# Kernel tuning notes

Hardware: AMD Instinct MI355X
Metric: run time of the kernel (lower is better)

Reference implementation:

```python
import jax, jax.numpy as jnp
import numpy as np

N = 100000      # nodes
E = 1600000     # edges (avg degree 16)
F_IN = 64       # input features
HID = 16        # ChebConv hidden (fixed in source)
C = 40          # num_classes
K = 2           # Chebyshev order (fixed in source)
LAMBDA_MAX = 2.0  # PyG ChebConv default


def setup_inputs() -> dict:
    key = jax.random.key(0)
    ks = jax.random.split(key, 6)
    x = jax.random.normal(ks[0], (N, F_IN), dtype=jnp.float32)
    edge_index = jax.random.randint(ks[1], (2, E), 0, N, dtype=jnp.int32)
    edge_weight = jax.random.uniform(ks[2], (E,), dtype=jnp.float32)
    W1 = jax.random.normal(ks[3], (K, F_IN, HID), dtype=jnp.float32) / np.float32(np.sqrt(F_IN))
    b1 = jnp.zeros((HID,), dtype=jnp.float32)
    W2 = jax.random.normal(ks[4], (K, HID, C), dtype=jnp.float32) / np.float32(np.sqrt(HID))
    b2 = jnp.zeros((C,), dtype=jnp.float32)
    return {"x": x, "edge_weight": edge_weight, "W1": W1, "b1": b1,
            "W2": W2, "b2": b2, "edge_index": edge_index}


def _cheb_norm(src, dst, edge_weight):
    # deg from symmetric normalization (aggregate at dst, PyG col)
    deg = jax.ops.segment_sum(edge_weight, dst, num_segments=N)
    dinv = jnp.where(deg > 0, jax.lax.rsqrt(jnp.maximum(deg, 1e-30)), 0.0)
    # Lhat = 2L/lambda_max - I ; with L = I - A_norm -> edge weight = -(2/lmax)*A_norm
    norm = -(2.0 / LAMBDA_MAX) * dinv[src] * edge_weight * dinv[dst]
    loop = 2.0 / LAMBDA_MAX - 1.0  # self-loop weight (0 for lambda_max=2)
    return norm, loop


def _cheb_conv(x, src, dst, norm, loop, W, b):
    # K=2: Tx0 = x, Tx1 = Lhat @ x (sparse gather-scale-scatter)
    Tx1 = jax.ops.segment_sum(norm[:, None] * x[src], dst, num_segments=N) + loop * x
    return jnp.einsum('nf,fo->no', x, W[0]) + jnp.einsum('nf,fo->no', Tx1, W[1]) + b


def reference(x, edge_weight, W1, b1, W2, b2, edge_index):
    src, dst = edge_index[0], edge_index[1]
    norm, loop = _cheb_norm(src, dst, edge_weight)
    h = jax.nn.relu(_cheb_conv(x, src, dst, norm, loop, W1, b1))
    # F.dropout with training=False is identity (inference reference)
    o = _cheb_conv(h, src, dst, norm, loop, W2, b2)
    return jax.nn.log_softmax(o, axis=1)
```

## Files before the change

### kernel.cpp

```cpp
#include <hip/hip_runtime.h>
#include <math.h>

#define NN 100000
#define NE 1600000
#define FIN 64
#define HID 16
#define NC 40

#define NG 512
#define GN 196
#define GCAP 3600
#define CH 4096
#define NBK ((NE + CH - 1) / CH)

typedef unsigned int u32;
typedef unsigned long long u64;
typedef unsigned short u16;

__device__ inline u16 f2bf(float f) {
    u32 u = __float_as_uint(f);
    return (u16)((u + 0x7FFF + ((u >> 16) & 1)) >> 16);
}
__device__ inline u32 pack2bf(float lo, float hi) {
    return (u32)f2bf(lo) | ((u32)f2bf(hi) << 16);
}

__global__ void k_zero(int* __restrict__ p) {
    p[blockIdx.x * 256 + threadIdx.x] = 0;
}

__global__ void __launch_bounds__(256) k_bucket(const int* __restrict__ src,
                                                const int* __restrict__ dst,
                                                const float* __restrict__ ew,
                                                int* __restrict__ bcur,
                                                u64* __restrict__ stg) {
    __shared__ u64 stage[CH];
    __shared__ int lcnt[NG];
    __shared__ int loff[NG];
    __shared__ int lcur[NG];
    __shared__ int gst[NG];
    __shared__ int ssum[256];
    __shared__ int totsh;
    int tid = threadIdx.x;
    int e0 = blockIdx.x * CH;
    for (int i = tid; i < NG; i += 256) lcnt[i] = 0;
    __syncthreads();
    u32 hb[16];
    #pragma unroll
    for (int k = 0; k < 16; ++k) {
        int e = e0 + k * 256 + tid;
        hb[k] = 0xFFFFFFFFu;
        if (e < NE) {
            int d = dst[e];
            int g = d / GN;
            hb[k] = ((u32)g << 16) | (u32)(d - g * GN);
            atomicAdd(&lcnt[g], 1);
        }
    }
    __syncthreads();
    int b0 = lcnt[2 * tid], b1c = lcnt[2 * tid + 1];
    int s = b0 + b1c;
    ssum[tid] = s;
    __syncthreads();
    #pragma unroll
    for (int off = 1; off < 256; off <<= 1) {
        int t = tid >= off ? ssum[tid - off] : 0;
        __syncthreads();
        ssum[tid] += t;
        __syncthreads();
    }
    int excl = ssum[tid] - s;
    loff[2 * tid] = excl;         loff[2 * tid + 1] = excl + b0;
    lcur[2 * tid] = excl;         lcur[2 * tid + 1] = excl + b0;
    gst[2 * tid]     = atomicAdd(&bcur[(2 * tid) << 4], b0);
    gst[2 * tid + 1] = atomicAdd(&bcur[(2 * tid + 1) << 4], b1c);
    if (tid == 255) totsh = ssum[255];
    __syncthreads();
    #pragma unroll
    for (int k = 0; k < 16; ++k) {
        if (hb[k] != 0xFFFFFFFFu) {
            int e = e0 + k * 256 + tid;
            int g = hb[k] >> 16;
            u32 q = (u32)fminf(ew[e] * 32767.f + 0.5f, 32767.f);
            u32 lo = (u32)src[e] | (q << 17);
            int slot = atomicAdd(&lcur[g], 1);
            stage[slot] = ((u64)hb[k] << 32) | (u64)lo;
        }
    }
    __syncthreads();
    int total = totsh;
    for (int i = tid; i < total; i += 256) {
        u64 r = stage[i];
        int g = (int)(r >> 48);
        int slot = gst[g] + (i - loff[g]);
        if (slot < GCAP) stg[(size_t)g * GCAP + slot] = r;
    }
}

__global__ void __launch_bounds__(256) k_build(const u64* __restrict__ stg,
                                               const int* __restrict__ bcur,
                                               int* __restrict__ row_ptr,
                                               float* __restrict__ dinv,
                                               u32* __restrict__ edges4) {
    __shared__ u64 lrec[GCAP];
    __shared__ u32 hc[GN];
    __shared__ u32 hw[GN];
    __shared__ int tsum[256];
    __shared__ int sb[NG];
    int g = blockIdx.x, tid = threadIdx.x;
    for (int i = tid; i < GN; i += 256) { hc[i] = 0; hw[i] = 0; }
    for (int i = tid; i < NG; i += 256) sb[i] = bcur[i << 4];
    __syncthreads();
    int n = sb[g];
    if (n > GCAP) n = GCAP;
    int b0 = sb[2 * tid], b1 = sb[2 * tid + 1];
    const u64* base = stg + (size_t)g * GCAP;
    for (int i = tid; i < n; i += 256) {
        u64 r = base[i];
        lrec[i] = r;
        int ld = (int)((r >> 32) & 0xFFFF);
        atomicAdd(&hc[ld], 1u);
        atomicAdd(&hw[ld], ((u32)r) >> 17);
    }
    __syncthreads();
    int s2 = b0 + b1;
    tsum[tid] = s2;
    __syncthreads();
    #pragma unroll
    for (int off = 1; off < 256; off <<= 1) {
        int t = tid >= off ? tsum[tid - off] : 0;
        __syncthreads();
        tsum[tid] += t;
        __syncthreads();
    }
    int excl = tsum[tid] - s2;
    sb[2 * tid] = excl; sb[2 * tid + 1] = excl + b0;
    __syncthreads();
    int gbase = sb[g];
    int c = (tid < GN) ? (int)hc[tid] : 0;
    tsum[tid] = c;
    __syncthreads();
    #pragma unroll
    for (int off = 1; off < 256; off <<= 1) {
        int t = tid >= off ? tsum[tid - off] : 0;
        __syncthreads();
        tsum[tid] += t;
        __syncthreads();
    }
    if (tid < GN) {
        int run = gbase + tsum[tid] - c;
        int nd = g * GN + tid;
        if (nd <= NN) {
            row_ptr[nd] = run;
            if (nd < NN) {
                float deg = (float)hw[tid] * (1.0f / 32767.0f);
                dinv[nd] = deg > 0.f ? rsqrtf(fmaxf(deg, 1e-30f)) : 0.f;
            }
        }
        hc[tid] = (u32)run;
    }
    __syncthreads();
    for (int i = tid; i < n; i += 256) {
        u64 r = lrec[i];
        int ld = (int)((r >> 32) & 0xFFFF);
        edges4[atomicAdd(&hc[ld], 1u)] = (u32)r;
    }
}

__global__ void __launch_bounds__(256) k_mm1(const float* __restrict__ x,
                                             const float* __restrict__ W1,
                                             const float* __restrict__ dinv,
                                             float* __restrict__ A1,
                                             u16* __restrict__ B0h) {
    __shared__ float4 w4[512];
    int tid = threadIdx.x;
    for (int i = tid; i < 512; i += 256) w4[i] = *(const float4*)(W1 + i * 4);
    __syncthreads();
    int sel = tid >> 7;
    int node = blockIdx.x * 128 + (tid & 127);
    if (node >= NN) return;
    const float4* xr = (const float4*)(x + node * FIN);
    const float4* wb = w4 + sel * 256;
    float4 a0 = {0,0,0,0}, a1 = {0,0,0,0}, a2 = {0,0,0,0}, a3 = {0,0,0,0};
    #pragma unroll
    for (int ft = 0; ft < 16; ++ft) {
        float4 xv = xr[ft];
        const float4* wf = wb + ft * 16;
        #pragma unroll
        for (int q = 0; q < 4; ++q) {
            float xs = q == 0 ? xv.x : q == 1 ? xv.y : q == 2 ? xv.z : xv.w;
            float4 w0 = wf[q * 4 + 0], w1v = wf[q * 4 + 1], w2v = wf[q * 4 + 2], w3v = wf[q * 4 + 3];
            a0.x += xs * w0.x; a0.y += xs * w0.y; a0.z += xs * w0.z; a0.w += xs * w0.w;
            a1.x += xs * w1v.x; a1.y += xs * w1v.y; a1.z += xs * w1v.z; a1.w += xs * w1v.w;
            a2.x += xs * w2v.x; a2.y += xs * w2v.y; a2.z += xs * w2v.z; a2.w += xs * w2v.w;
            a3.x += xs * w3v.x; a3.y += xs * w3v.y; a3.z += xs * w3v.z; a3.w += xs * w3v.w;
        }
    }
    if (sel == 0) {
        float4* o = (float4*)(A1 + node * HID);
        o[0] = a0; o[1] = a1; o[2] = a2; o[3] = a3;
    } else {
        float di = dinv[node];
        uint4 p0, p1;
        p0.x = pack2bf(a0.x * di, a0.y * di);
        p0.y = pack2bf(a0.z * di, a0.w * di);
        p0.z = pack2bf(a1.x * di, a1.y * di);
        p0.w = pack2bf(a1.z * di, a1.w * di);
        p1.x = pack2bf(a2.x * di, a2.y * di);
        p1.y = pack2bf(a2.z * di, a2.w * di);
        p1.z = pack2bf(a3.x * di, a3.y * di);
        p1.w = pack2bf(a3.z * di, a3.w * di);
        uint4* o = (uint4*)(B0h + node * HID);
        o[0] = p0; o[1] = p1;
    }
}

template <int MODE>
__global__ void k_gather(const int* __restrict__ row_ptr, const u32* __restrict__ edges4,
                         const u16* __restrict__ Bh,
                         const float* __restrict__ A1, const float* __restrict__ b1,
                         const float* __restrict__ dinv,
                         u32* __restrict__ o1, u32* __restrict__ o2) {
    int node = blockIdx.x * 4 + (threadIdx.x >> 6);
    int lane = threadIdx.x & 63;
    int slot = lane >> 3, q = lane & 7;
    if (node >= NN) return;
    int beg = row_ptr[node], end = row_ptr[node + 1];
    const u32* Bw = (const u32*)Bh;
    float accL = 0.f, accH = 0.f;
    int p0 = beg + slot;
    if (end - beg <= 16) {
        u32 r0 = (p0 < end) ? edges4[p0] : 0u;
        u32 r1 = (p0 + 8 < end) ? edges4[p0 + 8] : 0u;
        u32 c0 = Bw[(r0 & 0x1FFFF) * 8 + q];
        u32 c1 = Bw[(r1 & 0x1FFFF) * 8 + q];
        float w0 = (float)(r0 >> 17), w1 = (float)(r1 >> 17);
        accL = w0 * __uint_as_float(c0 << 16) + w1 * __uint_as_float(c1 << 16);
        accH = w0 * __uint_as_float(c0 & 0xFFFF0000u) + w1 * __uint_as_float(c1 & 0xFFFF0000u);
    } else {
        u32 r[4];
        #pragma unroll
        for (int k = 0; k < 4; ++k) {
            int p = p0 + 8 * k;
            r[k] = (p < end) ? edges4[p] : 0u;
        }
        #pragma unroll
        for (int k = 0; k < 4; ++k) {
            u32 c = Bw[(r[k] & 0x1FFFF) * 8 + q];
            float w = (float)(r[k] >> 17);
            accL += w * __uint_as_float(c << 16);
            accH += w * __uint_as_float(c & 0xFFFF0000u);
        }
        for (int p = p0 + 32; p < end; p += 8) {
            u32 rr = edges4[p];
            u32 c = Bw[(rr & 0x1FFFF) * 8 + q];
            float w = (float)(rr >> 17);
            accL += w * __uint_as_float(c << 16);
            accH += w * __uint_as_float(c & 0xFFFF0000u);
        }
    }
    #pragma unroll
    for (int m = 8; m < 64; m <<= 1) {
        accL += __shfl_xor(accL, m, 64);
        accH += __shfl_xor(accH, m, 64);
    }
    if (slot == 0) {
        float di = dinv[node];
        float sc = di * (1.0f / 32767.0f);
        int f = 2 * q;
        if (MODE == 0) {
            float2 a = *(const float2*)(A1 + node * HID + f);
            float2 bb = *(const float2*)(b1 + f);
            float hL = fmaxf(a.x - sc * accL + bb.x, 0.f);
            float hH = fmaxf(a.y - sc * accH + bb.y, 0.f);
            o1[node * 8 + q] = pack2bf(hL, hH);
            o2[node * 8 + q] = pack2bf(hL * di, hH * di);
        } else {
            o1[node * 8 + q] = pack2bf(-sc * accL, -sc * accH);
        }
    }
}

__global__ void __launch_bounds__(256) k_mm2_lsm(const u32* __restrict__ hb,
                                                 const u32* __restrict__ Tb,
                                                 const float* __restrict__ W2,
                                                 const float* __restrict__ b2,
                                                 float* __restrict__ out) {
    __shared__ float4 w4[32][10];
    __shared__ float sb2[NC];
    int tid = threadIdx.x;
    for (int i = tid; i < 320; i += 256) {
        int f = i / 10, ct = i % 10;
        w4[f][ct] = *(const float4*)(W2 + f * 40 + ct * 4);
    }
    for (int i = tid; i < NC; i += 256) sb2[i] = b2[i];
    __syncthreads();
    int node = blockIdx.x * 256 + tid;
    if (node >= NN) return;
    float v[32];
    uint4 ha = ((const uint4*)(hb + node * 8))[0];
    uint4 hbq = ((const uint4*)(hb + node * 8))[1];
    uint4 ta = ((const uint4*)(Tb + node * 8))[0];
    uint4 tbq = ((const uint4*)(Tb + node * 8))[1];
    u32 hw_[8] = {ha.x, ha.y, ha.z, ha.w, hbq.x, hbq.y, hbq.z, hbq.w};
    u32 tw_[8] = {ta.x, ta.y, ta.z, ta.w, tbq.x, tbq.y, tbq.z, tbq.w};
    #pragma unroll
    for (int qq = 0; qq < 8; ++qq) {
        v[2 * qq]     = __uint_as_float(hw_[qq] << 16);
        v[2 * qq + 1] = __uint_as_float(hw_[qq] & 0xFFFF0000u);
        v[16 + 2 * qq]     = __uint_as_float(tw_[qq] << 16);
        v[16 + 2 * qq + 1] = __uint_as_float(tw_[qq] & 0xFFFF0000u);
    }
    float lg[NC];
    #pragma unroll
    for (int ct = 0; ct < 10; ++ct) {
        float ax = sb2[ct * 4 + 0], ay = sb2[ct * 4 + 1], az = sb2[ct * 4 + 2], aw = sb2[ct * 4 + 3];
        #pragma unroll
        for (int f = 0; f < 32; ++f) {
            float4 wv = w4[f][ct];
            ax += v[f] * wv.x; ay += v[f] * wv.y; az += v[f] * wv.z; aw += v[f] * wv.w;
        }
        lg[ct * 4 + 0] = ax; lg[ct * 4 + 1] = ay; lg[ct * 4 + 2] = az; lg[ct * 4 + 3] = aw;
    }
    float m = lg[0];
    #pragma unroll
    for (int c = 1; c < NC; ++c) m = fmaxf(m, lg[c]);
    float sum = 0.f;
    #pragma unroll
    for (int c = 0; c < NC; ++c) sum += __expf(lg[c] - m);
    float lse = m + __logf(sum);
    float* orow = out + node * NC;
    #pragma unroll
    for (int ct = 0; ct < 10; ++ct) {
        float4 r;
        r.x = lg[ct * 4 + 0] - lse; r.y = lg[ct * 4 + 1] - lse;
        r.z = lg[ct * 4 + 2] - lse; r.w = lg[ct * 4 + 3] - lse;
        *(float4*)(orow + ct * 4) = r;
    }
}

extern "C" void kernel_launch(void* const* d_in, const int* in_sizes, int n_in,
                              void* d_out, int out_size, void* d_ws, size_t ws_size,
                              hipStream_t stream) {
    const float* x  = (const float*)d_in[0];
    const float* ew = (const float*)d_in[1];
    const float* W1 = (const float*)d_in[2];
    const float* b1 = (const float*)d_in[3];
    const float* W2 = (const float*)d_in[4];
    const float* b2 = (const float*)d_in[5];
    const int*   ei = (const int*)d_in[6];
    const int* src = ei;
    const int* dst = ei + NE;
    float* out = (float*)d_out;

    const int NPAD = 100352;
    int*   bcur    = (int*)d_ws;
    u64*   stg     = (u64*)(bcur + NG * 16);
    u32*   edges4  = (u32*)(stg + (size_t)NG * GCAP);
    int*   row_ptr = (int*)(edges4 + NE);
    float* dinv    = (float*)(row_ptr + NPAD);
    float* A1      = dinv + NPAD;
    u16*   B0h     = (u16*)(A1 + NN * HID);
    u32*   hbf     = (u32*)(B0h + NN * HID);
    u32*   h2      = hbf + NN * 8;
    u32*   Tbf     = h2 + NN * 8;

    k_zero<<<NG * 16 / 256, 256, 0, stream>>>(bcur);
    k_bucket<<<NBK, 256, 0, stream>>>(src, dst, ew, bcur, stg);
    k_build<<<NG, 256, 0, stream>>>(stg, bcur, row_ptr, dinv, edges4);
    k_mm1<<<(NN + 127) / 128, 256, 0, stream>>>(x, W1, dinv, A1, B0h);
    k_gather<0><<<(NN + 3) / 4, 256, 0, stream>>>(row_ptr, edges4, B0h, A1, b1, dinv, hbf, h2);
    k_gather<1><<<(NN + 3) / 4, 256, 0, stream>>>(row_ptr, edges4, (const u16*)h2, nullptr, nullptr, dinv, Tbf, nullptr);
    k_mm2_lsm<<<(NN + 255) / 256, 256, 0, stream>>>(hbf, Tbf, W2, b2, out);
}
```

Measured before the change: 133.4 us.

## Fuse second-layer gather with output matmul and log-softmax per wavefront

Merges the second sparse gather and the final W2 matmul plus log_softmax into one kernel. Each 64-lane wavefront handles one node: 8 lanes hold features, 8 slots split the 40 classes, and shuffles perform the reductions. This removes the Tbf intermediate round-trip through memory and one kernel launch. In exchange, every block reloads W2 into shared memory (25k blocks, 1280 floats each), adds shuffle reductions, and writes output as scattered 4-byte stores instead of float4.

```diff
diff --git a/kernel.cpp b/kernel.cpp
--- a/kernel.cpp
+++ b/kernel.cpp
@@ -215,12 +215,11 @@
     }
 }
 
-template <int MODE>
-__global__ void k_gather(const int* __restrict__ row_ptr, const u32* __restrict__ edges4,
-                         const u16* __restrict__ Bh,
-                         const float* __restrict__ A1, const float* __restrict__ b1,
-                         const float* __restrict__ dinv,
-                         u32* __restrict__ o1, u32* __restrict__ o2) {
+__global__ void k_gather0(const int* __restrict__ row_ptr, const u32* __restrict__ edges4,
+                          const u16* __restrict__ Bh,
+                          const float* __restrict__ A1, const float* __restrict__ b1,
+                          const float* __restrict__ dinv,
+                          u32* __restrict__ o1, u32* __restrict__ o2) {
     int node = blockIdx.x * 4 + (threadIdx.x >> 6);
     int lane = threadIdx.x & 63;
     int slot = lane >> 3, q = lane & 7;
@@ -268,75 +267,109 @@
         float di = dinv[node];
         float sc = di * (1.0f / 32767.0f);
         int f = 2 * q;
-        if (MODE == 0) {
-            float2 a = *(const float2*)(A1 + node * HID + f);
-            float2 bb = *(const float2*)(b1 + f);
-            float hL = fmaxf(a.x - sc * accL + bb.x, 0.f);
-            float hH = fmaxf(a.y - sc * accH + bb.y, 0.f);
-            o1[node * 8 + q] = pack2bf(hL, hH);
-            o2[node * 8 + q] = pack2bf(hL * di, hH * di);
-        } else {
-            o1[node * 8 + q] = pack2bf(-sc * accL, -sc * accH);
-        }
-    }
-}
-
-__global__ void __launch_bounds__(256) k_mm2_lsm(const u32* __restrict__ hb,
-                                                 const u32* __restrict__ Tb,
-                                                 const float* __restrict__ W2,
-                                                 const float* __restrict__ b2,
-                                                 float* __restrict__ out) {
-    __shared__ float4 w4[32][10];
-    __shared__ float sb2[NC];
+        float2 a = *(const float2*)(A1 + node * HID + f);
+        float2 bb = *(const float2*)(b1 + f);
+        float hL = fmaxf(a.x - sc * accL + bb.x, 0.f);
+        float hH = fmaxf(a.y - sc * accH + bb.y, 0.f);
+        o1[node * 8 + q] = pack2bf(hL, hH);
+        o2[node * 8 + q] = pack2bf(hL * di, hH * di);
+    }
+}
+
+__global__ void __launch_bounds__(256) k_gather_lsm(const int* __restrict__ row_ptr,
+                                                    const u32* __restrict__ edges4,
+                                                    const u16* __restrict__ Bh,
+                                                    const u32* __restrict__ hbf,
+                                                    const float* __restrict__ dinv,
+                                                    const float* __restrict__ W2,
+                                                    const float* __restrict__ b2,
+                                                    float* __restrict__ out) {
+    __shared__ float w2s[32 * 41];
+    __shared__ float b2s[NC];
     int tid = threadIdx.x;
-    for (int i = tid; i < 320; i += 256) {
-        int f = i / 10, ct = i % 10;
-        w4[f][ct] = *(const float4*)(W2 + f * 40 + ct * 4);
-    }
-    for (int i = tid; i < NC; i += 256) sb2[i] = b2[i];
-    __syncthreads();
-    int node = blockIdx.x * 256 + tid;
+    for (int i = tid; i < 1280; i += 256) {
+        int f = i / 40, c = i - f * 40;
+        w2s[f * 41 + c] = W2[i];
+    }
+    for (int i = tid; i < NC; i += 256) b2s[i] = b2[i];
+    __syncthreads();
+    int node = blockIdx.x * 4 + (tid >> 6);
+    int lane = tid & 63;
+    int slot = lane >> 3, q = lane & 7;
     if (node >= NN) return;
-    float v[32];
-    uint4 ha = ((const uint4*)(hb + node * 8))[0];
-    uint4 hbq = ((const uint4*)(hb + node * 8))[1];
-    uint4 ta = ((const uint4*)(Tb + node * 8))[0];
-    uint4 tbq = ((const uint4*)(Tb + node * 8))[1];
-    u32 hw_[8] = {ha.x, ha.y, ha.z, ha.w, hbq.x, hbq.y, hbq.z, hbq.w};
-    u32 tw_[8] = {ta.x, ta.y, ta.z, ta.w, tbq.x, tbq.y, tbq.z, tbq.w};
-    #pragma unroll
-    for (int qq = 0; qq < 8; ++qq) {
-        v[2 * qq]     = __uint_as_float(hw_[qq] << 16);
-        v[2 * qq + 1] = __uint_as_float(hw_[qq] & 0xFFFF0000u);
-        v[16 + 2 * qq]     = __uint_as_float(tw_[qq] << 16);
-        v[16 + 2 * qq + 1] = __uint_as_float(tw_[qq] & 0xFFFF0000u);
-    }
-    float lg[NC];
-    #pragma unroll
-    for (int ct = 0; ct < 10; ++ct) {
-        float ax = sb2[ct * 4 + 0], ay = sb2[ct * 4 + 1], az = sb2[ct * 4 + 2], aw = sb2[ct * 4 + 3];
-        #pragma unroll
-        for (int f = 0; f < 32; ++f) {
-            float4 wv = w4[f][ct];
-            ax += v[f] * wv.x; ay += v[f] * wv.y; az += v[f] * wv.z; aw += v[f] * wv.w;
-        }
-        lg[ct * 4 + 0] = ax; lg[ct * 4 + 1] = ay; lg[ct * 4 + 2] = az; lg[ct * 4 + 3] = aw;
-    }
-    float m = lg[0];
-    #pragma unroll
-    for (int c = 1; c < NC; ++c) m = fmaxf(m, lg[c]);
+    int beg = row_ptr[node], end = row_ptr[node + 1];
+    const u32* Bw = (const u32*)Bh;
+    float accL = 0.f, accH = 0.f;
+    int p0 = beg + slot;
+    if (end - beg <= 16) {
+        u32 r0 = (p0 < end) ? edges4[p0] : 0u;
+        u32 r1 = (p0 + 8 < end) ? edges4[p0 + 8] : 0u;
+        u32 c0 = Bw[(r0 & 0x1FFFF) * 8 + q];
+        u32 c1 = Bw[(r1 & 0x1FFFF) * 8 + q];
+        float w0 = (float)(r0 >> 17), w1 = (float)(r1 >> 17);
+        accL = w0 * __uint_as_float(c0 << 16) + w1 * __uint_as_float(c1 << 16);
+        accH = w0 * __uint_as_float(c0 & 0xFFFF0000u) + w1 * __uint_as_float(c1 & 0xFFFF0000u);
+    } else {
+        u32 r[4];
+        #pragma unroll
+        for (int k = 0; k < 4; ++k) {
+            int p = p0 + 8 * k;
+            r[k] = (p < end) ? edges4[p] : 0u;
+        }
+        #pragma unroll
+        for (int k = 0; k < 4; ++k) {
+            u32 c = Bw[(r[k] & 0x1FFFF) * 8 + q];
+            float w = (float)(r[k] >> 17);
+            accL += w * __uint_as_float(c << 16);
+            accH += w * __uint_as_float(c & 0xFFFF0000u);
+        }
+        for (int p = p0 + 32; p < end; p += 8) {
+            u32 rr = edges4[p];
+            u32 c = Bw[(rr & 0x1FFFF) * 8 + q];
+            float w = (float)(rr >> 17);
+            accL += w * __uint_as_float(c << 16);
+            accH += w * __uint_as_float(c & 0xFFFF0000u);
+        }
+    }
+    #pragma unroll
+    for (int m = 8; m < 64; m <<= 1) {
+        accL += __shfl_xor(accL, m, 64);
+        accH += __shfl_xor(accH, m, 64);
+    }
+    float di = dinv[node];
+    float sc = di * (1.0f / 32767.0f);
+    float t0 = -sc * accL, t1 = -sc * accH;
+    u32 hp = hbf[node * 8 + q];
+    float h0 = __uint_as_float(hp << 16);
+    float h1 = __uint_as_float(hp & 0xFFFF0000u);
+    int cb = 5 * slot;
+    const float* Wa0 = w2s + (2 * q) * 41 + cb;
+    const float* Wa1 = w2s + (2 * q + 1) * 41 + cb;
+    const float* Wb0 = w2s + (16 + 2 * q) * 41 + cb;
+    const float* Wb1 = w2s + (16 + 2 * q + 1) * 41 + cb;
+    float lg[5];
+    #pragma unroll
+    for (int i = 0; i < 5; ++i)
+        lg[i] = h0 * Wa0[i] + h1 * Wa1[i] + t0 * Wb0[i] + t1 * Wb1[i];
+    #pragma unroll
+    for (int m = 1; m < 8; m <<= 1) {
+        #pragma unroll
+        for (int i = 0; i < 5; ++i) lg[i] += __shfl_xor(lg[i], m, 64);
+    }
+    #pragma unroll
+    for (int i = 0; i < 5; ++i) lg[i] += b2s[cb + i];
+    float mx = lg[0];
+    #pragma unroll
+    for (int i = 1; i < 5; ++i) mx = fmaxf(mx, lg[i]);
+    #pragma unroll
+    for (int m = 8; m < 64; m <<= 1) mx = fmaxf(mx, __shfl_xor(mx, m, 64));
     float sum = 0.f;
     #pragma unroll
-    for (int c = 0; c < NC; ++c) sum += __expf(lg[c] - m);
-    float lse = m + __logf(sum);
-    float* orow = out + node * NC;
-    #pragma unroll
-    for (int ct = 0; ct < 10; ++ct) {
-        float4 r;
-        r.x = lg[ct * 4 + 0] - lse; r.y = lg[ct * 4 + 1] - lse;
-        r.z = lg[ct * 4 + 2] - lse; r.w = lg[ct * 4 + 3] - lse;
-        *(float4*)(orow + ct * 4) = r;
-    }
+    for (int i = 0; i < 5; ++i) sum += __expf(lg[i] - mx);
+    #pragma unroll
+    for (int m = 8; m < 64; m <<= 1) sum += __shfl_xor(sum, m, 64);
+    float lse = mx + __logf(sum);
+    if (q < 5) out[node * NC + cb + q] = lg[q] - lse;
 }
 
 extern "C" void kernel_launch(void* const* d_in, const int* in_sizes, int n_in,
@@ -363,13 +396,12 @@
     u16*   B0h     = (u16*)(A1 + NN * HID);
     u32*   hbf     = (u32*)(B0h + NN * HID);
     u32*   h2      = hbf + NN * 8;
-    u32*   Tbf     = h2 + NN * 8;
 
     k_zero<<<NG * 16 / 256, 256, 0, stream>>>(bcur);
     k_bucket<<<NBK, 256, 0, stream>>>(src, dst, ew, bcur, stg);
     k_build<<<NG, 256, 0, stream>>>(stg, bcur, row_ptr, dinv, edges4);
     k_mm1<<<(NN + 127) / 128, 256, 0, stream>>>(x, W1, dinv, A1, B0h);
-    k_gather<0><<<(NN + 3) / 4, 256, 0, stream>>>(row_ptr, edges4, B0h, A1, b1, dinv, hbf, h2);
-    k_gather<1><<<(NN + 3) / 4, 256, 0, stream>>>(row_ptr, edges4, (const u16*)h2, nullptr, nullptr, dinv, Tbf, nullptr);
-    k_mm2_lsm<<<(NN + 255) / 256, 256, 0, stream>>>(hbf, Tbf, W2, b2, out);
-}
+    k_gather0<<<(NN + 3) / 4, 256, 0, stream>>>(row_ptr, edges4, B0h, A1, b1, dinv, hbf, h2);
+    k_gather_lsm<<<(NN + 3) / 4, 256, 0, stream>>>(row_ptr, edges4, (const u16*)h2, hbf,
+                                                   dinv, W2, b2, out);
+}
```

Measured after the change: 146.4 us. 1.1x slower.
